# Kernel optimization log

Measured on AMD Instinct MI355X. Metric: run time of the kernel, lower is better.

## Reference

```python
import jax, jax.numpy as jnp
import numpy as np

N_HEADS = 8
STATE_TEMP = 0.5


def layer_norm(x, g, b, eps=1e-5):
    m = x.mean(-1, keepdims=True)
    v = ((x - m) ** 2).mean(-1, keepdims=True)
    return (x - m) / jnp.sqrt(v + eps) * g + b


def setup_inputs() -> dict:
    key = jax.random.key(0)
    ks = jax.random.split(key, 16)
    B, G, H, C, S, M, L = 2048, 10000, 256, 16, 32, 100, 3
    f32 = jnp.float32
    rn = lambda k, shape, scale: jax.random.normal(k, shape, f32) * scale
    return {
        'x': rn(ks[0], (B, G), 1.0),
        'enc_w1': rn(ks[1], (G, 2 * H), 1.0 / np.sqrt(G)),
        'enc_b1': jnp.zeros((2 * H,), f32),
        'enc_ln_g': jnp.ones((2 * H,), f32),
        'enc_ln_b': jnp.zeros((2 * H,), f32),
        'enc_w2': rn(ks[2], (2 * H, H), 1.0 / np.sqrt(2 * H)),
        'enc_b2': jnp.zeros((H,), f32),
        'mod_assign': rn(ks[3], (M, G), 1.0),
        'mod_inter': rn(ks[4], (M, M), 0.1) + jnp.eye(M, dtype=f32),
        'qkv_w': rn(ks[5], (L, H, 3 * H), 1.0 / np.sqrt(H)),
        'qkv_b': jnp.zeros((L, 3 * H), f32),
        'out_w': rn(ks[6], (L, H, H), 1.0 / np.sqrt(H)),
        'out_b': jnp.zeros((L, H), f32),
        'ln_g': jnp.ones((L, H), f32),
        'ln_b': jnp.zeros((L, H), f32),
        'prototypes': rn(ks[7], (S, H), 1.0),
        'clf_w1': rn(ks[8], (H, H // 2), 1.0 / np.sqrt(H)),
        'clf_b1': jnp.zeros((H // 2,), f32),
        'clf_w2': rn(ks[9], (H // 2, C), 1.0 / np.sqrt(H // 2)),
        'clf_b2': jnp.zeros((C,), f32),
        'marker_weights': jax.random.uniform(ks[10], (C, G), f32),
    }


def reference(x, enc_w1, enc_b1, enc_ln_g, enc_ln_b, enc_w2, enc_b2,
              mod_assign, mod_inter, qkv_w, qkv_b, out_w, out_b, ln_g, ln_b,
              prototypes, clf_w1, clf_b1, clf_w2, clf_b2, marker_weights):
    B = x.shape[0]
    Hd = enc_w2.shape[1]
    hd = Hd // N_HEADS
    # --- gene encoder (Linear -> LN -> ReLU -> Linear), dropout off (eval) ---
    h = jax.nn.relu(layer_norm(x @ enc_w1 + enc_b1, enc_ln_g, enc_ln_b))
    gene_features = h @ enc_w2 + enc_b2  # [B, Hd]
    # --- gene regulatory module (only sparsity_loss feeds the output dict) ---
    module_weights = jax.nn.softmax(mod_assign, axis=1)  # [M, G]
    sparsity_loss = jnp.mean(jnp.abs(module_weights)) * 0.01
    # --- stacked biological attention over seq_len N = 1 ---
    f = gene_features[:, None, :]  # [B, 1, Hd]
    for i in range(qkv_w.shape[0]):
        residual = f
        qkv = (f @ qkv_w[i] + qkv_b[i]).reshape(B, 1, 3, N_HEADS, hd)
        qkv = qkv.transpose(2, 0, 3, 1, 4)  # [3, B, nh, 1, hd]
        q, k, v = qkv[0], qkv[1], qkv[2]
        # N=1 != n_genes so the interaction-mask branch is skipped
        attn = jax.nn.softmax((q @ k.swapaxes(-2, -1)) * hd ** -0.5, axis=-1)
        o = (attn @ v).swapaxes(1, 2).reshape(B, 1, Hd)
        o = o @ out_w[i] + out_b[i]
        f = layer_norm(o + residual, ln_g[i], ln_b[i])
    feats = f[:, 0]  # [B, Hd]
    # --- soft assignment to cell-state prototypes via cosine similarity ---
    fn = jnp.linalg.norm(feats, axis=-1, keepdims=True)  # [B, 1]
    pn = jnp.linalg.norm(prototypes, axis=-1)            # [S]
    sim = (feats @ prototypes.T) / jnp.maximum(fn * pn[None, :], 1e-8)
    state_weights = jax.nn.softmax(sim / STATE_TEMP, axis=1)
    cell_states = state_weights @ prototypes  # [B, Hd]
    # --- classifier head ---
    logits = jax.nn.relu(cell_states @ clf_w1 + clf_b1) @ clf_w2 + clf_b2
    # --- eval-mode marker scores from buffer ---
    C, G = marker_weights.shape
    marker_scores = jnp.broadcast_to(marker_weights[None], (B, C, G))
    denom = jnp.maximum(jnp.sum(jnp.abs(marker_weights), axis=1, keepdims=True), 1e-12)
    marker_importance = marker_weights / denom
    return (logits, cell_states, sparsity_loss, marker_scores, marker_importance)
```

## Files before the change

### kernel.cpp

```cpp
#include <hip/hip_runtime.h>
#include <stdint.h>

#define GG 10000
#define H2 512
#define KP 10240
#define KCH 1280
#define KSTEPS 40

#define O_CS 32768L
#define O_SP 557056L
#define O_MS 557057L
#define O_MI 328237057L

typedef __attribute__((ext_vector_type(8))) short v8s;
typedef __attribute__((ext_vector_type(4))) float v4f;
typedef __attribute__((ext_vector_type(4))) unsigned short u16x4;
typedef __attribute__((ext_vector_type(8))) unsigned short u16x8;

__device__ __forceinline__ unsigned short bf16_rne(float f){
  unsigned u = __float_as_uint(f);
  u += 0x7fffu + ((u>>16)&1u);
  return (unsigned short)(u>>16);
}
__device__ __forceinline__ float bf16_f(unsigned short h){
  return __uint_as_float(((unsigned)h)<<16);
}

#define GL16(g,l) __builtin_amdgcn_global_load_lds( \
    (__attribute__((address_space(1))) void*)(uintptr_t)(g), \
    (__attribute__((address_space(3))) void*)(l), 16, 0, 0)

__global__ __launch_bounds__(256) void k_split_x(const float* __restrict__ x,
    unsigned short* __restrict__ xh, unsigned short* __restrict__ xl){
  int idx = blockIdx.x*256 + threadIdx.x;
  int row = idx / (KP/4);
  int k = (idx - row*(KP/4))*4;
  float4 v = make_float4(0.f,0.f,0.f,0.f);
  if (k < GG) v = *(const float4*)(x + (long)row*GG + k);
  float c[4] = {v.x,v.y,v.z,v.w};
  u16x4 hv, lv;
  #pragma unroll
  for (int j=0;j<4;j++){
    unsigned short h = bf16_rne(c[j]);
    hv[j] = h;
    lv[j] = bf16_rne(c[j] - bf16_f(h));
  }
  long off = (long)row*KP + k;
  *(u16x4*)(xh+off) = hv;
  *(u16x4*)(xl+off) = lv;
}

__global__ __launch_bounds__(256) void k_split_w1t(const float* __restrict__ w1,
    unsigned short* __restrict__ wth, unsigned short* __restrict__ wtl){
  __shared__ unsigned T[64][65];
  int k0 = blockIdx.x*64, n0 = blockIdx.y*64;
  int tid = threadIdx.x;
  {
    int kr = tid>>2, nc = (tid&3)*16;
    int kk = k0 + kr;
    #pragma unroll
    for (int j=0;j<16;j+=4){
      float4 v = make_float4(0.f,0.f,0.f,0.f);
      if (kk < GG) v = *(const float4*)(w1 + (long)kk*H2 + n0 + nc + j);
      float c[4] = {v.x,v.y,v.z,v.w};
      #pragma unroll
      for (int jj=0;jj<4;jj++){
        unsigned short h = bf16_rne(c[jj]);
        unsigned short l = bf16_rne(c[jj] - bf16_f(h));
        T[kr][nc+j+jj] = (unsigned)h | ((unsigned)l<<16);
      }
    }
  }
  __syncthreads();
  {
    int n = tid>>2, kc = (tid&3)*16;
    u16x8 h0, h1, l0, l1;
    #pragma unroll
    for (int j=0;j<8;j++){
      unsigned a = T[kc+j][n];
      unsigned b = T[kc+8+j][n];
      h0[j] = (unsigned short)(a & 0xffffu); l0[j] = (unsigned short)(a>>16);
      h1[j] = (unsigned short)(b & 0xffffu); l1[j] = (unsigned short)(b>>16);
    }
    long off = (long)(n0+n)*KP + k0 + kc;
    *(u16x8*)(wth+off)   = h0; *(u16x8*)(wth+off+8) = h1;
    *(u16x8*)(wtl+off)   = l0; *(u16x8*)(wtl+off+8) = l1;
  }
}

__global__ __launch_bounds__(256) void k_gemm1(
    const unsigned short* __restrict__ xh, const unsigned short* __restrict__ xl,
    const unsigned short* __restrict__ wth, const unsigned short* __restrict__ wtl,
    float* __restrict__ pc){
  __shared__ unsigned short Ah[4096], Al[4096], Bh[4096], Bl[4096];
  const int tid = threadIdx.x;
  const int wid = tid>>6, lane = tid&63;
  const int bm = blockIdx.x, bn = blockIdx.y, kz = blockIdx.z;
  const int c0 = wid*2, c1 = c0+1;
  const int srow = lane>>2;
  const int sk8 = (lane&3)*8;
  const long kb0 = (long)kz*KCH + sk8;
  const long rA0 = (long)(bm*128 + c0*16 + srow)*KP + kb0;
  const long rA1 = (long)(bm*128 + c1*16 + srow)*KP + kb0;
  const long rB0 = (long)(bn*128 + c0*16 + srow)*KP + kb0;
  const long rB1 = (long)(bn*128 + c1*16 + srow)*KP + kb0;
  const unsigned short* pAh0 = xh + rA0;  const unsigned short* pAh1 = xh + rA1;
  const unsigned short* pAl0 = xl + rA0;  const unsigned short* pAl1 = xl + rA1;
  const unsigned short* pBh0 = wth + rB0; const unsigned short* pBh1 = wth + rB1;
  const unsigned short* pBl0 = wtl + rB0; const unsigned short* pBl1 = wtl + rB1;
  unsigned short* dAh0 = &Ah[c0*512]; unsigned short* dAh1 = &Ah[c1*512];
  unsigned short* dAl0 = &Al[c0*512]; unsigned short* dAl1 = &Al[c1*512];
  unsigned short* dBh0 = &Bh[c0*512]; unsigned short* dBh1 = &Bh[c1*512];
  unsigned short* dBl0 = &Bl[c0*512]; unsigned short* dBl1 = &Bl[c1*512];
  const int wr = wid>>1, wc = wid&1;
  const int fr = lane&15, fq = lane>>4;
  v4f acc[4][4];
  #pragma unroll
  for (int m=0;m<4;m++)
    #pragma unroll
    for (int n=0;n<4;n++){ v4f z = {0.f,0.f,0.f,0.f}; acc[m][n] = z; }

  for (int s=0; s<KSTEPS; ++s){
    GL16(pAh0, dAh0); GL16(pAh1, dAh1);
    GL16(pAl0, dAl0); GL16(pAl1, dAl1);
    GL16(pBh0, dBh0); GL16(pBh1, dBh1);
    GL16(pBl0, dBl0); GL16(pBl1, dBl1);
    pAh0 += 32; pAh1 += 32; pAl0 += 32; pAl1 += 32;
    pBh0 += 32; pBh1 += 32; pBl0 += 32; pBl1 += 32;
    __syncthreads();
    v8s ah[4], al[4], bh[4], bl[4];
    #pragma unroll
    for (int m=0;m<4;m++){
      int off = (wr*64 + m*16 + fr)*32 + fq*8;
      ah[m] = *(const v8s*)&Ah[off];
      al[m] = *(const v8s*)&Al[off];
    }
    #pragma unroll
    for (int n=0;n<4;n++){
      int off = (wc*64 + n*16 + fr)*32 + fq*8;
      bh[n] = *(const v8s*)&Bh[off];
      bl[n] = *(const v8s*)&Bl[off];
    }
    #pragma unroll
    for (int m=0;m<4;m++)
      #pragma unroll
      for (int n=0;n<4;n++){
        acc[m][n] = __builtin_amdgcn_mfma_f32_16x16x32_bf16(ah[m], bh[n], acc[m][n], 0,0,0);
        acc[m][n] = __builtin_amdgcn_mfma_f32_16x16x32_bf16(ah[m], bl[n], acc[m][n], 0,0,0);
        acc[m][n] = __builtin_amdgcn_mfma_f32_16x16x32_bf16(al[m], bh[n], acc[m][n], 0,0,0);
      }
    __syncthreads();
  }
  float* op = pc + (long)kz*(2048L*512L);
  #pragma unroll
  for (int m=0;m<4;m++){
    #pragma unroll
    for (int n=0;n<4;n++){
      int col = bn*128 + wc*64 + n*16 + fr;
      #pragma unroll
      for (int r=0;r<4;r++){
        int row = bm*128 + wr*64 + m*16 + fq*4 + r;
        op[(long)row*512 + col] = acc[m][n][r];
      }
    }
  }
}

__global__ __launch_bounds__(256) void k_reduce_ln(const float* __restrict__ pc,
    const float* __restrict__ b1, const float* __restrict__ g, const float* __restrict__ b,
    float* __restrict__ t1){
  __shared__ float red[8];
  int row = blockIdx.x, tid = threadIdx.x;
  long base = (long)row*512;
  float v0 = b1[tid], v1 = b1[tid+256];
  #pragma unroll
  for (int kz=0;kz<8;kz++){
    v0 += pc[(long)kz*1048576 + base + tid];
    v1 += pc[(long)kz*1048576 + base + tid + 256];
  }
  float s = v0+v1, q = v0*v0 + v1*v1;
  #pragma unroll
  for (int off=32; off; off>>=1){ s += __shfl_xor(s, off); q += __shfl_xor(q, off); }
  if ((tid&63)==0){ red[tid>>6] = s; red[4+(tid>>6)] = q; }
  __syncthreads();
  float sum = red[0]+red[1]+red[2]+red[3];
  float ssq = red[4]+red[5]+red[6]+red[7];
  float mean = sum*(1.f/512.f);
  float var  = ssq*(1.f/512.f) - mean*mean;
  float rstd = rsqrtf(var + 1e-5f);
  float r0 = (v0-mean)*rstd*g[tid]     + b[tid];
  float r1 = (v1-mean)*rstd*g[tid+256] + b[tid+256];
  t1[base+tid]     = fmaxf(r0, 0.f);
  t1[base+tid+256] = fmaxf(r1, 0.f);
}

__global__ __launch_bounds__(256) void k_gemm_f32(
    const float* __restrict__ A, int lda,
    const float* __restrict__ W, int ldw,
    const float* __restrict__ bias,
    float* __restrict__ C, int ldo, int K){
  __shared__ float As[64][36];
  __shared__ float WsT[64][36];
  const int tid = threadIdx.x;
  const int bx = blockIdx.x, by = blockIdx.y;
  const int tx = tid&15, ty = tid>>4;
  const int ar = tid>>2, ak = (tid&3)*8;
  const int wr2 = tid>>3, wc2 = (tid&7)*8;
  float acc[4][4];
  #pragma unroll
  for (int i=0;i<4;i++)
    #pragma unroll
    for (int j=0;j<4;j++) acc[i][j] = 0.f;
  for (int kb=0; kb<K; kb+=32){
    float4 a0 = *(const float4*)(A + (long)(bx*64+ar)*lda + kb + ak);
    float4 a1 = *(const float4*)(A + (long)(bx*64+ar)*lda + kb + ak + 4);
    float4 w0 = *(const float4*)(W + (long)(kb+wr2)*ldw + by*64 + wc2);
    float4 w1v= *(const float4*)(W + (long)(kb+wr2)*ldw + by*64 + wc2 + 4);
    __syncthreads();
    *(float4*)&As[ar][ak]   = a0;
    *(float4*)&As[ar][ak+4] = a1;
    float cw[8] = {w0.x,w0.y,w0.z,w0.w,w1v.x,w1v.y,w1v.z,w1v.w};
    #pragma unroll
    for (int jj=0;jj<8;jj++) WsT[wc2+jj][wr2] = cw[jj];
    __syncthreads();
    #pragma unroll
    for (int k4=0;k4<8;k4++){
      float4 av[4], wv[4];
      #pragma unroll
      for (int i=0;i<4;i++) av[i] = *(const float4*)&As[ty + i*16][k4*4];
      #pragma unroll
      for (int j=0;j<4;j++) wv[j] = *(const float4*)&WsT[tx + j*16][k4*4];
      #pragma unroll
      for (int i=0;i<4;i++)
        #pragma unroll
        for (int j=0;j<4;j++)
          acc[i][j] += av[i].x*wv[j].x + av[i].y*wv[j].y + av[i].z*wv[j].z + av[i].w*wv[j].w;
    }
  }
  #pragma unroll
  for (int i=0;i<4;i++){
    int r = bx*64 + ty + i*16;
    #pragma unroll
    for (int j=0;j<4;j++){
      int c = by*64 + tx + j*16;
      C[(long)r*ldo + c] = acc[i][j] + bias[c];
    }
  }
}

__global__ __launch_bounds__(256) void k_add_ln(const float* __restrict__ o,
    const float* __restrict__ res, const float* __restrict__ g, const float* __restrict__ b,
    float* __restrict__ fout){
  __shared__ float red[8];
  int row = blockIdx.x, tid = threadIdx.x;
  long base = (long)row*256;
  float x = o[base+tid] + res[base+tid];
  float s = x, q = x*x;
  #pragma unroll
  for (int off=32; off; off>>=1){ s += __shfl_xor(s, off); q += __shfl_xor(q, off); }
  if ((tid&63)==0){ red[tid>>6] = s; red[4+(tid>>6)] = q; }
  __syncthreads();
  float sum = red[0]+red[1]+red[2]+red[3];
  float ssq = red[4]+red[5]+red[6]+red[7];
  float mean = sum*(1.f/256.f);
  float var  = ssq*(1.f/256.f) - mean*mean;
  float rstd = rsqrtf(var + 1e-5f);
  fout[base+tid] = (x-mean)*rstd*g[tid] + b[tid];
}

__global__ __launch_bounds__(256) void k_head(const float* __restrict__ f,
    const float* __restrict__ protos, const float* __restrict__ w1, const float* __restrict__ b1,
    const float* __restrict__ w2, const float* __restrict__ b2,
    float* __restrict__ logits, float* __restrict__ cs_out){
  __shared__ float ff[256], csb[256], hid[128], simr[32], pnl[32], sw[32], red[8];
  int row = blockIdx.x, tid = threadIdx.x;
  float fv = f[(long)row*256 + tid];
  ff[tid] = fv;
  float s = fv*fv;
  #pragma unroll
  for (int off=32; off; off>>=1) s += __shfl_xor(s, off);
  if ((tid&63)==0) red[tid>>6] = s;
  __syncthreads();
  float fn = sqrtf(red[0]+red[1]+red[2]+red[3]);
  int p = tid>>3, e = tid&7;
  float d = 0.f, q = 0.f;
  for (int k=e*32; k<e*32+32; k++){ float pv = protos[p*256+k]; d += ff[k]*pv; q += pv*pv; }
  d += __shfl_xor(d,1); q += __shfl_xor(q,1);
  d += __shfl_xor(d,2); q += __shfl_xor(q,2);
  d += __shfl_xor(d,4); q += __shfl_xor(q,4);
  if (e==0){ simr[p] = d; pnl[p] = sqrtf(q); }
  __syncthreads();
  if (tid < 64){
    float z = (tid<32) ? (2.f*simr[tid]/fmaxf(fn*pnl[tid], 1e-8f)) : -3e38f;
    float m = z;
    #pragma unroll
    for (int off=16; off; off>>=1) m = fmaxf(m, __shfl_xor(m, off));
    float ev = (tid<32) ? expf(z - m) : 0.f;
    float sm = ev;
    #pragma unroll
    for (int off=16; off; off>>=1) sm += __shfl_xor(sm, off);
    if (tid<32) sw[tid] = ev/sm;
  }
  __syncthreads();
  float cs = 0.f;
  #pragma unroll 8
  for (int pp=0;pp<32;pp++) cs += sw[pp]*protos[pp*256+tid];
  cs_out[(long)row*256+tid] = cs;
  csb[tid] = cs;
  __syncthreads();
  if (tid<128){
    float hv = b1[tid];
    for (int k=0;k<256;k++) hv += csb[k]*w1[k*128+tid];
    hid[tid] = fmaxf(hv, 0.f);
  }
  __syncthreads();
  if (tid<16){
    float lv = b2[tid];
    for (int j=0;j<128;j++) lv += hid[j]*w2[j*16+tid];
    logits[(long)row*16+tid] = lv;
  }
}

__global__ void k_misc(float* __restrict__ out){
  if (threadIdx.x==0 && blockIdx.x==0) out[O_SP] = 0.01f/10000.0f;
}

__global__ __launch_bounds__(256) void k_fill_marker(const float* __restrict__ mw,
    float* __restrict__ out){
  int b = blockIdx.y;
  int t = blockIdx.x*256 + threadIdx.x;
  float* base = out + O_MS + (long)b*160000;
  if (t < 40000){
    int i = 4*t;
    float4 A  = *(const float4*)(mw + i);
    float4 Bv = (i+4 < 160000) ? *(const float4*)(mw + i + 4) : *(const float4*)(mw);
    float4 v = make_float4(A.w, Bv.x, Bv.y, Bv.z);
    *(float4*)(base + 3 + i) = v;
  }
  if (b==0 && t<3) base[t] = mw[t];
}

__global__ __launch_bounds__(256) void k_importance(const float* __restrict__ mw,
    float* __restrict__ out){
  __shared__ float red[4];
  int c = blockIdx.x, tid = threadIdx.x;
  float s = 0.f;
  for (int g0=tid; g0<10000; g0+=256) s += fabsf(mw[c*10000+g0]);
  #pragma unroll
  for (int off=32; off; off>>=1) s += __shfl_xor(s, off);
  if ((tid&63)==0) red[tid>>6] = s;
  __syncthreads();
  float inv = 1.f/fmaxf(red[0]+red[1]+red[2]+red[3], 1e-12f);
  for (int g0=tid; g0<10000; g0+=256)
    out[O_MI + (long)c*10000 + g0] = mw[c*10000+g0]*inv;
}

extern "C" void kernel_launch(void* const* d_in, const int* in_sizes, int n_in,
                              void* d_out, int out_size, void* d_ws, size_t ws_size,
                              hipStream_t stream){
  const float* x        = (const float*)d_in[0];
  const float* enc_w1   = (const float*)d_in[1];
  const float* enc_b1   = (const float*)d_in[2];
  const float* enc_ln_g = (const float*)d_in[3];
  const float* enc_ln_b = (const float*)d_in[4];
  const float* enc_w2   = (const float*)d_in[5];
  const float* enc_b2   = (const float*)d_in[6];
  const float* qkv_w    = (const float*)d_in[9];
  const float* qkv_b    = (const float*)d_in[10];
  const float* out_w    = (const float*)d_in[11];
  const float* out_b    = (const float*)d_in[12];
  const float* ln_g     = (const float*)d_in[13];
  const float* ln_b     = (const float*)d_in[14];
  const float* protos   = (const float*)d_in[15];
  const float* clf_w1   = (const float*)d_in[16];
  const float* clf_b1   = (const float*)d_in[17];
  const float* clf_w2   = (const float*)d_in[18];
  const float* clf_b2   = (const float*)d_in[19];
  const float* mw       = (const float*)d_in[20];
  float* out = (float*)d_out;

  char* scr = (char*)(((uintptr_t)d_out + O_MS*4 + 255) & ~(uintptr_t)255);
  unsigned short* xh  = (unsigned short*)(scr);
  unsigned short* xl  = (unsigned short*)(scr + 41943040L);
  unsigned short* wth = (unsigned short*)(scr + 83886080L);
  unsigned short* wtl = (unsigned short*)(scr + 94371840L);
  float* pc = (float*)(scr + 104857600L);
  float* t1 = (float*)(scr + 138412032L);
  float* f0 = (float*)(scr + 142606336L);
  float* f1 = (float*)(scr + 144703488L);
  float* vb = (float*)(scr + 146800640L);
  float* ob = (float*)(scr + 148897792L);

  k_split_x  <<<20480, 256, 0, stream>>>(x, xh, xl);
  k_split_w1t<<<dim3(160, 8), 256, 0, stream>>>(enc_w1, wth, wtl);
  k_gemm1    <<<dim3(16, 4, 8), 256, 0, stream>>>(xh, xl, wth, wtl, pc);
  k_reduce_ln<<<2048, 256, 0, stream>>>(pc, enc_b1, enc_ln_g, enc_ln_b, t1);
  k_gemm_f32 <<<dim3(32, 4), 256, 0, stream>>>(t1, 512, enc_w2, 256, enc_b2, f0, 256, 512);
  const float* fin = f0; float* fo = f1;
  for (int i=0;i<3;i++){
    k_gemm_f32<<<dim3(32,4), 256, 0, stream>>>(fin, 256, qkv_w + (long)i*196608 + 512, 768,
                                               qkv_b + i*768 + 512, vb, 256, 256);
    k_gemm_f32<<<dim3(32,4), 256, 0, stream>>>(vb, 256, out_w + (long)i*65536, 256,
                                               out_b + i*256, ob, 256, 256);
    k_add_ln  <<<2048, 256, 0, stream>>>(ob, fin, ln_g + i*256, ln_b + i*256, fo);
    const float* tmp = fo; fo = (float*)fin; fin = tmp;
  }
  k_head<<<2048, 256, 0, stream>>>(fin, protos, clf_w1, clf_b1, clf_w2, clf_b2,
                                   out, out + O_CS);
  k_misc<<<1, 64, 0, stream>>>(out);
  k_fill_marker<<<dim3(157, 2048), 256, 0, stream>>>(mw, out);
  k_importance <<<16, 256, 0, stream>>>(mw, out);
}
```

Before: 592.3 us.

## Fold V and output projections, fuse LN, overlap marker fill with compute

With a sequence length of one, attention reduces to the V projection, so the V and output weights are pre-multiplied into a single combined matrix and bias. Each layer then becomes one row-blocked GEMM with the residual add and LayerNorm fused in. The large broadcast marker_scores write, which is bandwidth-bound, is split into chunks and interleaved into the GEMM1, row-GEMM and head kernels so the stores overlap with compute. A small tail kernel finishes the rest. This cuts launches and separate memory-bound passes, but the chunk offsets are intricate and rounding changes slightly because of the weight pre-multiplication.

```diff
diff --git a/kernel.cpp b/kernel.cpp
--- a/kernel.cpp
+++ b/kernel.cpp
@@ -11,6 +11,15 @@
 #define O_SP 557056L
 #define O_MS 557057L
 #define O_MI 328237057L
+#define NM   327680000L
+
+#define FB_G1   0L
+#define FC_G1   52428800L
+#define FB_G2   52428800L
+#define FB_L0   55574528L
+#define FB_H    61865984L
+#define FB_TAIL 71696384L
+#define T4_END  81919999L
 
 typedef __attribute__((ext_vector_type(8))) short v8s;
 typedef __attribute__((ext_vector_type(4))) float v4f;
@@ -29,6 +38,82 @@
 #define GL16(g,l) __builtin_amdgcn_global_load_lds( \
     (__attribute__((address_space(1))) void*)(uintptr_t)(g), \
     (__attribute__((address_space(3))) void*)(l), 16, 0, 0)
+
+__global__ __launch_bounds__(256) void k_prep(const float* __restrict__ mw,
+    const float* __restrict__ qkv_b, const float* __restrict__ out_w,
+    const float* __restrict__ out_b, float* __restrict__ mws2,
+    float* __restrict__ bc, float* __restrict__ out){
+  int bid = blockIdx.x, tid = threadIdx.x;
+  if (bid < 1250){
+    int j = bid*256 + tid;
+    int s = j + 3;
+    if (s >= 160000) s -= 160000;
+    if (s >= 160000) s -= 160000;
+    mws2[j] = mw[s];
+  } else if (bid < 1253){
+    int i = bid - 1250;
+    float acc = out_b[i*256 + tid];
+    const float* wo = out_w + (long)i*65536;
+    const float* qb = qkv_b + i*768 + 512;
+    for (int j=0;j<256;j++) acc += qb[j]*wo[j*256+tid];
+    bc[i*256+tid] = acc;
+  } else {
+    if (tid==0) out[O_SP] = 0.01f/10000.0f;
+  }
+}
+
+__global__ __launch_bounds__(256) void k_combine(const float* __restrict__ qkv_w,
+    const float* __restrict__ out_w, float* __restrict__ Wc){
+  __shared__ float As[64][36];
+  __shared__ float WsT[64][36];
+  const int z = blockIdx.z;
+  const float* A = qkv_w + (long)z*196608 + 512;
+  const float* W = out_w + (long)z*65536;
+  float* C = Wc + (long)z*65536;
+  const int tid = threadIdx.x;
+  const int bx = blockIdx.x, by = blockIdx.y;
+  const int tx = tid&15, ty = tid>>4;
+  const int ar = tid>>2, ak = (tid&3)*8;
+  const int wr2 = tid>>3, wc2 = (tid&7)*8;
+  float acc[4][4];
+  #pragma unroll
+  for (int i=0;i<4;i++)
+    #pragma unroll
+    for (int j=0;j<4;j++) acc[i][j] = 0.f;
+  for (int kb=0; kb<256; kb+=32){
+    float4 a0 = *(const float4*)(A + (long)(bx*64+ar)*768 + kb + ak);
+    float4 a1 = *(const float4*)(A + (long)(bx*64+ar)*768 + kb + ak + 4);
+    float4 w0 = *(const float4*)(W + (long)(kb+wr2)*256 + by*64 + wc2);
+    float4 w1v= *(const float4*)(W + (long)(kb+wr2)*256 + by*64 + wc2 + 4);
+    __syncthreads();
+    *(float4*)&As[ar][ak]   = a0;
+    *(float4*)&As[ar][ak+4] = a1;
+    float cw[8] = {w0.x,w0.y,w0.z,w0.w,w1v.x,w1v.y,w1v.z,w1v.w};
+    #pragma unroll
+    for (int jj=0;jj<8;jj++) WsT[wc2+jj][wr2] = cw[jj];
+    __syncthreads();
+    #pragma unroll
+    for (int k4=0;k4<8;k4++){
+      float4 av[4], wv[4];
+      #pragma unroll
+      for (int i=0;i<4;i++) av[i] = *(const float4*)&As[ty + i*16][k4*4];
+      #pragma unroll
+      for (int j=0;j<4;j++) wv[j] = *(const float4*)&WsT[tx + j*16][k4*4];
+      #pragma unroll
+      for (int i=0;i<4;i++)
+        #pragma unroll
+        for (int j=0;j<4;j++)
+          acc[i][j] += av[i].x*wv[j].x + av[i].y*wv[j].y + av[i].z*wv[j].z + av[i].w*wv[j].w;
+    }
+  }
+  #pragma unroll
+  for (int i=0;i<4;i++){
+    int r = bx*64 + ty + i*16;
+    #pragma unroll
+    for (int j=0;j<4;j++)
+      C[(long)r*256 + by*64 + tx + j*16] = acc[i][j];
+  }
+}
 
 __global__ __launch_bounds__(256) void k_split_x(const float* __restrict__ x,
     unsigned short* __restrict__ xh, unsigned short* __restrict__ xl){
@@ -91,7 +176,7 @@
 __global__ __launch_bounds__(256) void k_gemm1(
     const unsigned short* __restrict__ xh, const unsigned short* __restrict__ xl,
     const unsigned short* __restrict__ wth, const unsigned short* __restrict__ wtl,
-    float* __restrict__ pc){
+    float* __restrict__ pc, const float* __restrict__ mws2, float* __restrict__ outp){
   __shared__ unsigned short Ah[4096], Al[4096], Bh[4096], Bl[4096];
   const int tid = threadIdx.x;
   const int wid = tid>>6, lane = tid&63;
@@ -114,6 +199,10 @@
   unsigned short* dBl0 = &Bl[c0*512]; unsigned short* dBl1 = &Bl[c1*512];
   const int wr = wid>>1, wc = wid&1;
   const int fr = lane&15, fq = lane>>4;
+  const int blockflat = (int)blockIdx.x + 16*((int)blockIdx.y + 4*(int)blockIdx.z);
+  const long ft0 = (long)blockflat*102400 + (long)tid*10;
+  int fm = (int)((4*ft0) % 160000);
+  float* fst = outp + O_MS + 3 + 4*ft0;
   v4f acc[4][4];
   #pragma unroll
   for (int m=0;m<4;m++)
@@ -127,6 +216,16 @@
     GL16(pBl0, dBl0); GL16(pBl1, dBl1);
     pAh0 += 32; pAh1 += 32; pAl0 += 32; pAl1 += 32;
     pBh0 += 32; pBh1 += 32; pBl0 += 32; pBl1 += 32;
+    #pragma unroll
+    for (int h=0; h<2; ++h){
+      float4 fv[5];
+      #pragma unroll
+      for (int u=0;u<5;u++) fv[u] = *(const float4*)(mws2 + fm + h*20 + 4*u);
+      #pragma unroll
+      for (int u=0;u<5;u++) *(float4*)(fst + h*20 + 4*u) = fv[u];
+    }
+    fm += 10240; if (fm >= 160000) fm -= 160000;
+    fst += 10240;
     __syncthreads();
     v8s ah[4], al[4], bh[4], bl[4];
     #pragma unroll
@@ -194,84 +293,86 @@
   t1[base+tid+256] = fmaxf(r1, 0.f);
 }
 
-__global__ __launch_bounds__(256) void k_gemm_f32(
-    const float* __restrict__ A, int lda,
-    const float* __restrict__ W, int ldw,
-    const float* __restrict__ bias,
-    float* __restrict__ C, int ldo, int K){
-  __shared__ float As[64][36];
-  __shared__ float WsT[64][36];
+__global__ __launch_bounds__(256) void k_rowgemm(
+    const float* __restrict__ A, const float* __restrict__ W,
+    const float* __restrict__ bias, const float* __restrict__ g, const float* __restrict__ b,
+    float* __restrict__ out, int K, int doLN,
+    const float* __restrict__ msrc, float* __restrict__ mout, long fillbase, int F4){
+  __shared__ float As[8][512];
+  __shared__ float Ws[32][256];
+  __shared__ float rs[8][4], rq[8][4];
   const int tid = threadIdx.x;
-  const int bx = blockIdx.x, by = blockIdx.y;
-  const int tx = tid&15, ty = tid>>4;
-  const int ar = tid>>2, ak = (tid&3)*8;
-  const int wr2 = tid>>3, wc2 = (tid&7)*8;
-  float acc[4][4];
-  #pragma unroll
-  for (int i=0;i<4;i++)
-    #pragma unroll
-    for (int j=0;j<4;j++) acc[i][j] = 0.f;
-  for (int kb=0; kb<K; kb+=32){
-    float4 a0 = *(const float4*)(A + (long)(bx*64+ar)*lda + kb + ak);
-    float4 a1 = *(const float4*)(A + (long)(bx*64+ar)*lda + kb + ak + 4);
-    float4 w0 = *(const float4*)(W + (long)(kb+wr2)*ldw + by*64 + wc2);
-    float4 w1v= *(const float4*)(W + (long)(kb+wr2)*ldw + by*64 + wc2 + 4);
-    __syncthreads();
-    *(float4*)&As[ar][ak]   = a0;
-    *(float4*)&As[ar][ak+4] = a1;
-    float cw[8] = {w0.x,w0.y,w0.z,w0.w,w1v.x,w1v.y,w1v.z,w1v.w};
-    #pragma unroll
-    for (int jj=0;jj<8;jj++) WsT[wc2+jj][wr2] = cw[jj];
-    __syncthreads();
-    #pragma unroll
-    for (int k4=0;k4<8;k4++){
-      float4 av[4], wv[4];
-      #pragma unroll
-      for (int i=0;i<4;i++) av[i] = *(const float4*)&As[ty + i*16][k4*4];
-      #pragma unroll
-      for (int j=0;j<4;j++) wv[j] = *(const float4*)&WsT[tx + j*16][k4*4];
-      #pragma unroll
-      for (int i=0;i<4;i++)
-        #pragma unroll
-        for (int j=0;j<4;j++)
-          acc[i][j] += av[i].x*wv[j].x + av[i].y*wv[j].y + av[i].z*wv[j].z + av[i].w*wv[j].w;
-    }
-  }
-  #pragma unroll
-  for (int i=0;i<4;i++){
-    int r = bx*64 + ty + i*16;
-    #pragma unroll
-    for (int j=0;j<4;j++){
-      int c = by*64 + tx + j*16;
-      C[(long)r*ldo + c] = acc[i][j] + bias[c];
-    }
-  }
-}
-
-__global__ __launch_bounds__(256) void k_add_ln(const float* __restrict__ o,
-    const float* __restrict__ res, const float* __restrict__ g, const float* __restrict__ b,
-    float* __restrict__ fout){
-  __shared__ float red[8];
-  int row = blockIdx.x, tid = threadIdx.x;
-  long base = (long)row*256;
-  float x = o[base+tid] + res[base+tid];
-  float s = x, q = x*x;
-  #pragma unroll
-  for (int off=32; off; off>>=1){ s += __shfl_xor(s, off); q += __shfl_xor(q, off); }
-  if ((tid&63)==0){ red[tid>>6] = s; red[4+(tid>>6)] = q; }
-  __syncthreads();
-  float sum = red[0]+red[1]+red[2]+red[3];
-  float ssq = red[4]+red[5]+red[6]+red[7];
-  float mean = sum*(1.f/256.f);
-  float var  = ssq*(1.f/256.f) - mean*mean;
-  float rstd = rsqrtf(var + 1e-5f);
-  fout[base+tid] = (x-mean)*rstd*g[tid] + b[tid];
+  const long r0 = (long)blockIdx.x * 8;
+  const int kq = K>>2;
+  for (int p = tid; p < 2*K; p += 256){
+    int row = p / kq;
+    int c4 = (p - row*kq)*4;
+    *(float4*)&As[row][c4] = *(const float4*)(A + (r0+row)*K + c4);
+  }
+  float acc[8] = {0.f,0.f,0.f,0.f,0.f,0.f,0.f,0.f};
+  const int nc = K>>5;
+  const long ft0 = fillbase + (long)blockIdx.x*((long)nc*256*F4) + (long)tid*F4;
+  int fm = (int)((4*ft0) % 160000);
+  float* fst = mout + 3 + 4*ft0;
+  const int fmstep = 1024*F4;
+  __syncthreads();
+  for (int c = 0; c < nc; ++c){
+    const float* Wb = W + (long)(c*32)*256;
+    #pragma unroll
+    for (int u=0; u<8; u++){
+      int p2 = u*256 + tid;
+      int j = p2 >> 6, c4 = (p2 & 63)*4;
+      *(float4*)&Ws[j][c4] = *(const float4*)(Wb + j*256 + c4);
+    }
+    for (int u=0; u<F4; u++)
+      *(float4*)(fst + 4*u) = *(const float4*)(msrc + fm + 4*u);
+    fm += fmstep; if (fm >= 160000) fm -= 160000;
+    fst += fmstep;
+    __syncthreads();
+    #pragma unroll
+    for (int j=0;j<32;j++){
+      float wv = Ws[j][tid];
+      int kk = c*32 + j;
+      #pragma unroll
+      for (int r=0;r<8;r++) acc[r] += As[r][kk]*wv;
+    }
+    __syncthreads();
+  }
+  float bv = bias[tid];
+  if (doLN){
+    float xv[8];
+    #pragma unroll
+    for (int r=0;r<8;r++) xv[r] = acc[r] + bv + As[r][tid];
+    int w = tid>>6, lane = tid&63;
+    #pragma unroll
+    for (int r=0;r<8;r++){
+      float s = xv[r], q = xv[r]*xv[r];
+      #pragma unroll
+      for (int off=32; off; off>>=1){ s += __shfl_xor(s,off); q += __shfl_xor(q,off); }
+      if (lane==0){ rs[r][w] = s; rq[r][w] = q; }
+    }
+    __syncthreads();
+    float gv = g[tid], bbv = b[tid];
+    #pragma unroll
+    for (int r=0;r<8;r++){
+      float sum = rs[r][0]+rs[r][1]+rs[r][2]+rs[r][3];
+      float ssq = rq[r][0]+rq[r][1]+rq[r][2]+rq[r][3];
+      float mean = sum*(1.f/256.f);
+      float var  = ssq*(1.f/256.f) - mean*mean;
+      float rstd = rsqrtf(var + 1e-5f);
+      out[(r0+r)*256 + tid] = (xv[r]-mean)*rstd*gv + bbv;
+    }
+  } else {
+    #pragma unroll
+    for (int r=0;r<8;r++) out[(r0+r)*256 + tid] = acc[r] + bv;
+  }
 }
 
 __global__ __launch_bounds__(256) void k_head(const float* __restrict__ f,
     const float* __restrict__ protos, const float* __restrict__ w1, const float* __restrict__ b1,
     const float* __restrict__ w2, const float* __restrict__ b2,
-    float* __restrict__ logits, float* __restrict__ cs_out){
+    float* __restrict__ logits, float* __restrict__ cs_out,
+    const float* __restrict__ msrc, float* __restrict__ mout){
   __shared__ float ff[256], csb[256], hid[128], simr[32], pnl[32], sw[32], red[8];
   int row = blockIdx.x, tid = threadIdx.x;
   float fv = f[(long)row*256 + tid];
@@ -319,25 +420,15 @@
     for (int j=0;j<128;j++) lv += hid[j]*w2[j*16+tid];
     logits[(long)row*16+tid] = lv;
   }
-}
-
-__global__ void k_misc(float* __restrict__ out){
-  if (threadIdx.x==0 && blockIdx.x==0) out[O_SP] = 0.01f/10000.0f;
-}
-
-__global__ __launch_bounds__(256) void k_fill_marker(const float* __restrict__ mw,
-    float* __restrict__ out){
-  int b = blockIdx.y;
-  int t = blockIdx.x*256 + threadIdx.x;
-  float* base = out + O_MS + (long)b*160000;
-  if (t < 40000){
-    int i = 4*t;
-    float4 A  = *(const float4*)(mw + i);
-    float4 Bv = (i+4 < 160000) ? *(const float4*)(mw + i + 4) : *(const float4*)(mw);
-    float4 v = make_float4(A.w, Bv.x, Bv.y, Bv.z);
-    *(float4*)(base + 3 + i) = v;
-  }
-  if (b==0 && t<3) base[t] = mw[t];
+  long hb0 = FB_H + (long)row * 4800;
+  int fm = (int)((4*hb0 + 4*(long)tid) % 160000);
+  float* fp = mout + 3 + 4*hb0 + 4*(long)tid;
+  #pragma unroll 4
+  for (int u=0; u<19; u++){
+    if (u*256 + tid < 4800)
+      *(float4*)(fp + (long)u*1024) = *(const float4*)(msrc + fm);
+    fm += 1024; if (fm >= 160000) fm -= 160000;
+  }
 }
 
 __global__ __launch_bounds__(256) void k_importance(const float* __restrict__ mw,
@@ -353,6 +444,27 @@
   float inv = 1.f/fmaxf(red[0]+red[1]+red[2]+red[3], 1e-12f);
   for (int g0=tid; g0<10000; g0+=256)
     out[O_MI + (long)c*10000 + g0] = mw[c*10000+g0]*inv;
+}
+
+__global__ __launch_bounds__(256) void k_fill_tail(const float* __restrict__ mw,
+    float* __restrict__ out){
+  long idx = (long)blockIdx.x*256 + threadIdx.x;
+  #pragma unroll 4
+  for (int u=0; u<8; u++){
+    long t = FB_TAIL + idx + (long)u*1277952;
+    if (t < T4_END){
+      long ee = 3 + 4*t;
+      int i = (int)(ee % 160000);
+      float4 A = *(const float4*)(mw + i - 3);
+      int ib = i+1; if (ib >= 160000) ib = 0;
+      float4 B = *(const float4*)(mw + ib);
+      *(float4*)(out + O_MS + ee) = make_float4(A.w, B.x, B.y, B.z);
+    }
+  }
+  if (blockIdx.x==0 && threadIdx.x<4){
+    if (threadIdx.x<3) out[O_MS + threadIdx.x] = mw[threadIdx.x];
+    else out[O_MS + 327679999L] = mw[159999];
+  }
 }
 
 extern "C" void kernel_launch(void* const* d_in, const int* in_sizes, int n_in,
@@ -379,35 +491,36 @@
   const float* mw       = (const float*)d_in[20];
   float* out = (float*)d_out;
 
-  char* scr = (char*)(((uintptr_t)d_out + O_MS*4 + 255) & ~(uintptr_t)255);
+  char* scr = (char*)(((uintptr_t)d_out + (uintptr_t)(O_MS + 287680000L)*4 + 255) & ~(uintptr_t)255);
   unsigned short* xh  = (unsigned short*)(scr);
   unsigned short* xl  = (unsigned short*)(scr + 41943040L);
   unsigned short* wth = (unsigned short*)(scr + 83886080L);
   unsigned short* wtl = (unsigned short*)(scr + 94371840L);
-  float* pc = (float*)(scr + 104857600L);
-  float* t1 = (float*)(scr + 138412032L);
-  float* f0 = (float*)(scr + 142606336L);
-  float* f1 = (float*)(scr + 144703488L);
-  float* vb = (float*)(scr + 146800640L);
-  float* ob = (float*)(scr + 148897792L);
-
+  float* pc   = (float*)(scr + 104857600L);
+  float* t1   = (float*)(scr + 138412032L);
+  float* f0   = (float*)(scr + 142606336L);
+  float* f1   = (float*)(scr + 144703488L);
+  float* mws2 = (float*)(scr + 146800640L);
+  float* Wc   = (float*)(scr + 148080640L);
+  float* bc   = (float*)(scr + 148867072L);
+
+  k_prep     <<<1254, 256, 0, stream>>>(mw, qkv_b, out_w, out_b, mws2, bc, out);
+  k_combine  <<<dim3(4,4,3), 256, 0, stream>>>(qkv_w, out_w, Wc);
   k_split_x  <<<20480, 256, 0, stream>>>(x, xh, xl);
   k_split_w1t<<<dim3(160, 8), 256, 0, stream>>>(enc_w1, wth, wtl);
-  k_gemm1    <<<dim3(16, 4, 8), 256, 0, stream>>>(xh, xl, wth, wtl, pc);
+  k_gemm1    <<<dim3(16, 4, 8), 256, 0, stream>>>(xh, xl, wth, wtl, pc, mws2, out);
   k_reduce_ln<<<2048, 256, 0, stream>>>(pc, enc_b1, enc_ln_g, enc_ln_b, t1);
-  k_gemm_f32 <<<dim3(32, 4), 256, 0, stream>>>(t1, 512, enc_w2, 256, enc_b2, f0, 256, 512);
+  k_rowgemm  <<<256, 256, 0, stream>>>(t1, enc_w2, enc_b2, enc_ln_g, enc_ln_b,
+                                       f0, 512, 0, mws2, out + O_MS, FB_G2, 3);
   const float* fin = f0; float* fo = f1;
   for (int i=0;i<3;i++){
-    k_gemm_f32<<<dim3(32,4), 256, 0, stream>>>(fin, 256, qkv_w + (long)i*196608 + 512, 768,
-                                               qkv_b + i*768 + 512, vb, 256, 256);
-    k_gemm_f32<<<dim3(32,4), 256, 0, stream>>>(vb, 256, out_w + (long)i*65536, 256,
-                                               out_b + i*256, ob, 256, 256);
-    k_add_ln  <<<2048, 256, 0, stream>>>(ob, fin, ln_g + i*256, ln_b + i*256, fo);
+    k_rowgemm<<<256, 256, 0, stream>>>(fin, Wc + (long)i*65536, bc + i*256,
+                                       ln_g + i*256, ln_b + i*256, fo, 256, 1,
+                                       mws2, out + O_MS, FB_L0 + (long)i*2097152L, 4);
     const float* tmp = fo; fo = (float*)fin; fin = tmp;
   }
-  k_head<<<2048, 256, 0, stream>>>(fin, protos, clf_w1, clf_b1, clf_w2, clf_b2,
-                                   out, out + O_CS);
-  k_misc<<<1, 64, 0, stream>>>(out);
-  k_fill_marker<<<dim3(157, 2048), 256, 0, stream>>>(mw, out);
-  k_importance <<<16, 256, 0, stream>>>(mw, out);
-}
+  k_head     <<<2048, 256, 0, stream>>>(fin, protos, clf_w1, clf_b1, clf_w2, clf_b2,
+                                        out, out + O_CS, mws2, out + O_MS);
+  k_importance<<<16, 256, 0, stream>>>(mw, out);
+  k_fill_tail<<<4992, 256, 0, stream>>>(mw, out);
+}
```

Result: slower. 737.5 us (+24.5%).
